# Kernel tuning notes

Measured on AMD Instinct MI355X. Metric: run time of the kernel, lower is better.

The kernel has to match this reference:

```python
import jax, jax.numpy as jnp
import numpy as np

EPS = 1e-09
TOP_K = 2
TEMPERATURE = 1.0


def setup_inputs() -> dict:
    key = jax.random.key(0)
    k1, k2, k3, k4 = jax.random.split(key, 4)
    B, T, H, C, E = 16, 8192, 256, 256, 16
    D = H + C          # router input dim = 512
    F = 2 * D          # hidden dim of router MLP = 1024
    inputs = jax.random.normal(k1, (B, T, H), dtype=jnp.float32)
    cond = jax.random.normal(k2, (B, T, C), dtype=jnp.float32)
    # router params (torch init: normal(0, 0.02) weights, zero bias)
    W1 = 0.02 * jax.random.normal(k3, (D, F), dtype=jnp.float32)
    b1 = jnp.zeros((F,), dtype=jnp.float32)
    W2 = 0.02 * jax.random.normal(k4, (F, E), dtype=jnp.float32)
    b2 = jnp.zeros((E,), dtype=jnp.float32)
    return {"inputs": inputs, "cond": cond, "W1": W1, "b1": b1, "W2": W2, "b2": b2}


def reference(inputs, cond, W1, b1, W2, b2):
    B, T, H = inputs.shape
    E = W2.shape[-1]
    # --- logits: concat(inputs, cond) -> Linear -> GELU(exact) -> Linear ---
    x = jnp.concatenate([inputs, cond], axis=-1).reshape(-1, H + cond.shape[-1])  # [N, D]
    h = jax.nn.gelu(x @ W1 + b1, approximate=False)                               # [N, F]
    logits = h @ W2 + b2                                                          # [N, E]
    # --- probabilities: max-subtract / temperature, softmax, clamp ---
    logits = (logits - jnp.max(logits, axis=-1, keepdims=True)) / TEMPERATURE
    probs = jax.nn.softmax(logits, axis=-1)
    probs = jnp.clip(probs, EPS, 1.0 - EPS)                                       # [N, E]
    # --- deterministic top-k selection (use_argmax / eval mode) ---
    top_vals, top_idx = jax.lax.top_k(probs, TOP_K)                               # [N, K]
    onehot = jax.nn.one_hot(top_idx, E, dtype=probs.dtype)                        # [N, K, E]
    router_mask = jnp.sum(onehot, axis=1)                                         # [N, E] 0/1
    router_probs = jnp.einsum('nke,nk->ne', onehot, top_vals)                     # scatter top-k probs
    # --- normalize selected probs ---
    router_probs = router_probs / jnp.sum(router_probs, axis=-1, keepdims=True)
    router_mask = router_mask.reshape(B, T, E)
    top_idx = top_idx.reshape(B, T, TOP_K)
    router_probs = router_probs.reshape(B, T, E)
    probs_full = probs.reshape(B, T, E)
    return (router_mask, top_idx, router_probs, probs_full)
```

## Files before the change

### kernel.cpp

```cpp
#include <hip/hip_runtime.h>
#include <math.h>

#define NTOK 131072
#define HDIM 256
#define DDIM 512
#define FDIM 1024
#define EDIM 16
#define TBLK 128
#define FCH  128
#define KST  32
#define HSS  68

#define WS_XL   134217728ULL
#define WS_W1H  268435456ULL
#define WS_W1L  269484032ULL
#define WS_NEED 270532608ULL

typedef __attribute__((ext_vector_type(8))) _Float16 v8h;
typedef __attribute__((ext_vector_type(4))) _Float16 v4h;
typedef __attribute__((ext_vector_type(4))) float v4f;

__device__ __forceinline__ void f2h2(float v, _Float16& h, _Float16& l) {
    h = (_Float16)v;
    l = (_Float16)(v - (float)h);
}

__device__ __forceinline__ void pack8(const float* u, v8h& hh, v8h& hl) {
    _Float16 h0,l0,h1,l1,h2,l2,h3,l3,h4,l4,h5,l5,h6,l6,h7,l7;
    f2h2(u[0],h0,l0); f2h2(u[1],h1,l1); f2h2(u[2],h2,l2); f2h2(u[3],h3,l3);
    f2h2(u[4],h4,l4); f2h2(u[5],h5,l5); f2h2(u[6],h6,l6); f2h2(u[7],h7,l7);
    hh[0]=h0; hh[1]=h1; hh[2]=h2; hh[3]=h3; hh[4]=h4; hh[5]=h5; hh[6]=h6; hh[7]=h7;
    hl[0]=l0; hl[1]=l1; hl[2]=l2; hl[3]=l3; hl[4]=l4; hl[5]=l5; hl[6]=l6; hl[7]=l7;
}

__device__ __forceinline__ void gl16(const void* g, void* l) {
    __builtin_amdgcn_global_load_lds(
        (const __attribute__((address_space(1))) void*)g,
        (__attribute__((address_space(3))) void*)l, 16, 0, 0);
}

__global__ __launch_bounds__(256, 4)
void prep_x(const float* __restrict__ inp, const float* __restrict__ cnd,
            _Float16* __restrict__ xh, _Float16* __restrict__ xl)
{
    const size_t g = (size_t)blockIdx.x * 256 + threadIdx.x;
    const int lane = (int)(g & 63);
    const int fg   = (int)((g >> 6) & 7);
    const int T    = (int)(g >> 9);
    const int tb = T >> 4, st = T & 15;
    const int tok = tb * TBLK + fg * 16 + (lane & 15);
    const int k   = st * KST + (lane >> 4) * 8;
    const float* src = (k < HDIM) ? (inp + (size_t)tok * HDIM + k)
                                  : (cnd + (size_t)tok * HDIM + (k - HDIM));
    float u[8];
    *(float4*)&u[0] = *(const float4*)(src);
    *(float4*)&u[4] = *(const float4*)(src + 4);
    v8h hh, hl;
    pack8(u, hh, hl);
    *(v8h*)(xh + g * 8) = hh;
    *(v8h*)(xl + g * 8) = hl;
}

__global__ __launch_bounds__(256, 4)
void prep_w1(const float* __restrict__ W1,
             _Float16* __restrict__ wh, _Float16* __restrict__ wl)
{
    const int g = blockIdx.x * 256 + threadIdx.x;
    const int lane = g & 63;
    const int K = (g >> 6) & 15;
    const int F = g >> 10;
    const int f  = F * 16 + (lane & 15);
    const int kb = K * KST + (lane >> 4) * 8;
    float u[8];
#pragma unroll
    for (int e = 0; e < 8; ++e)
        u[e] = W1[(size_t)(kb + e) * FDIM + f];
    v8h hh, hl;
    pack8(u, hh, hl);
    *(v8h*)(wh + (size_t)g * 8) = hh;
    *(v8h*)(wl + (size_t)g * 8) = hl;
}

__global__ __launch_bounds__(256, 2)
void router_mfma12(const _Float16* __restrict__ xh, const _Float16* __restrict__ xl,
                   const _Float16* __restrict__ w1h, const _Float16* __restrict__ w1l,
                   const float* __restrict__ b1,
                   const float* __restrict__ W2,
                   const float* __restrict__ b2,
                   float* __restrict__ out)
{
    __shared__ __align__(16) char smem[34816];
    _Float16* xs_h = (_Float16*)(smem);
    _Float16* xs_l = (_Float16*)(smem + 8192);
    _Float16* ws_h = (_Float16*)(smem + 16384);
    _Float16* ws_l = (_Float16*)(smem + 24576);
    _Float16* hs_h = (_Float16*)(smem);
    _Float16* hs_l = (_Float16*)(smem + 17408);

    const int tid  = threadIdx.x;
    const int lane = tid & 63;
    const int w    = tid >> 6;
    const int wr   = w >> 1;
    const int wf   = w & 1;
    const int l15  = lane & 15;
    const int l4   = lane >> 4;
    const int t0   = blockIdx.x * TBLK;

    const float b2v = b2[l15];
    v4f accL[2] = {{0.f,0.f,0.f,0.f},{0.f,0.f,0.f,0.f}};

    for (int fc = 0; fc < FDIM; fc += FCH) {
        v4f acc[4][4];
#pragma unroll
        for (int mf = 0; mf < 4; ++mf)
#pragma unroll
            for (int nf = 0; nf < 4; ++nf)
                acc[mf][nf] = (v4f){0.f,0.f,0.f,0.f};

        for (int st = 0; st < 16; ++st) {
            __syncthreads();
            {
                const char* sh = (const char*)(xh + ((size_t)blockIdx.x * 16 + st) * 4096);
                const char* sl = (const char*)(xl + ((size_t)blockIdx.x * 16 + st) * 4096);
                gl16(sh + tid * 16,        smem + tid * 16);
                gl16(sh + tid * 16 + 4096, smem + tid * 16 + 4096);
                gl16(sl + tid * 16,        smem + 8192 + tid * 16);
                gl16(sl + tid * 16 + 4096, smem + 8192 + tid * 16 + 4096);
                const size_t wb0 = (((size_t)((fc >> 4) + (tid >> 6)) * 16 + st) * 64
                                    + (tid & 63)) * 16;
                const size_t wb1 = (((size_t)((fc >> 4) + 4 + (tid >> 6)) * 16 + st) * 64
                                    + (tid & 63)) * 16;
                gl16((const char*)w1h + wb0, smem + 16384 + tid * 16);
                gl16((const char*)w1h + wb1, smem + 16384 + tid * 16 + 4096);
                gl16((const char*)w1l + wb0, smem + 24576 + tid * 16);
                gl16((const char*)w1l + wb1, smem + 24576 + tid * 16 + 4096);
            }
            __syncthreads();
            {
                v8h ah[4], al[4];
#pragma unroll
                for (int mf = 0; mf < 4; ++mf) {
                    const int aoff = ((4 * wr + mf) * 64 + lane) * 8;
                    ah[mf] = *(const v8h*)(xs_h + aoff);
                    al[mf] = *(const v8h*)(xs_l + aoff);
                }
#pragma unroll
                for (int nf = 0; nf < 4; ++nf) {
                    const int boff = ((4 * wf + nf) * 64 + lane) * 8;
                    const v8h bh = *(const v8h*)(ws_h + boff);
                    const v8h bl = *(const v8h*)(ws_l + boff);
#pragma unroll
                    for (int mf = 0; mf < 4; ++mf) {
                        acc[mf][nf] = __builtin_amdgcn_mfma_f32_16x16x32_f16(ah[mf], bh, acc[mf][nf], 0, 0, 0);
                        acc[mf][nf] = __builtin_amdgcn_mfma_f32_16x16x32_f16(al[mf], bh, acc[mf][nf], 0, 0, 0);
                        acc[mf][nf] = __builtin_amdgcn_mfma_f32_16x16x32_f16(ah[mf], bl, acc[mf][nf], 0, 0, 0);
                    }
                }
            }
        }
        __syncthreads();

        float b1v[4];
#pragma unroll
        for (int nf = 0; nf < 4; ++nf)
            b1v[nf] = b1[fc + 64 * wf + 16 * nf + l15];

#pragma unroll
        for (int h = 0; h < 2; ++h) {
            if (wf == h) {
#pragma unroll
                for (int mf = 0; mf < 4; ++mf)
#pragma unroll
                    for (int nf = 0; nf < 4; ++nf)
#pragma unroll
                        for (int r = 0; r < 4; ++r) {
                            const float v = acc[mf][nf][r] + b1v[nf];
                            const float gl = 0.5f * v * (1.0f + erff(v * 0.70710678118654752f));
                            _Float16 hh, hl;
                            f2h2(gl, hh, hl);
                            const int tok  = 64 * wr + 16 * mf + 4 * l4 + r;
                            const int fcol = 16 * nf + l15;
                            hs_h[tok * HSS + fcol] = hh;
                            hs_l[tok * HSS + fcol] = hl;
                        }
            }
            __syncthreads();
#pragma unroll
            for (int ks = 0; ks < 2; ++ks) {
                v8h vbh, vbl;
#pragma unroll
                for (int j = 0; j < 8; ++j) {
                    const float u = W2[(size_t)(fc + 64 * h + 32 * ks + 8 * l4 + j) * EDIM + l15];
                    _Float16 hh, hl;
                    f2h2(u, hh, hl);
                    vbh[j] = hh; vbl[j] = hl;
                }
#pragma unroll
                for (int mf2 = 0; mf2 < 2; ++mf2) {
                    const int aoff = (32 * w + 16 * mf2 + l15) * HSS + 32 * ks + 8 * l4;
                    const v8h vah = *(const v8h*)(hs_h + aoff);
                    const v8h val = *(const v8h*)(hs_l + aoff);
                    accL[mf2] = __builtin_amdgcn_mfma_f32_16x16x32_f16(vah, vbh, accL[mf2], 0, 0, 0);
                    accL[mf2] = __builtin_amdgcn_mfma_f32_16x16x32_f16(val, vbh, accL[mf2], 0, 0, 0);
                    accL[mf2] = __builtin_amdgcn_mfma_f32_16x16x32_f16(vah, vbl, accL[mf2], 0, 0, 0);
                }
            }
            if (h == 0) __syncthreads();
        }
    }

    float lg[8];
#pragma unroll
    for (int mf2 = 0; mf2 < 2; ++mf2)
#pragma unroll
        for (int r = 0; r < 4; ++r)
            lg[mf2 * 4 + r] = accL[mf2][r] + b2v;

    const int tx = l15;
#pragma unroll
    for (int i = 0; i < 8; ++i) {
        const int t = t0 + 32 * w + 16 * (i >> 2) + 4 * l4 + (i & 3);
        float mx = lg[i];
#pragma unroll
        for (int m = 1; m < 16; m <<= 1) mx = fmaxf(mx, __shfl_xor(mx, m, 64));
        float p = expf(lg[i] - mx);
        float s = p;
#pragma unroll
        for (int m = 1; m < 16; m <<= 1) s += __shfl_xor(s, m, 64);
        float pr = p / s;
        pr = fminf(fmaxf(pr, 1e-9f), 1.0f - 1e-9f);

        float v1 = pr; int i1 = tx;
#pragma unroll
        for (int m = 1; m < 16; m <<= 1) {
            const float vo = __shfl_xor(v1, m, 64);
            const int   io = __shfl_xor(i1, m, 64);
            if (vo > v1 || (vo == v1 && io < i1)) { v1 = vo; i1 = io; }
        }
        float v2 = (tx == i1) ? -1.0f : pr; int i2 = tx;
#pragma unroll
        for (int m = 1; m < 16; m <<= 1) {
            const float vo = __shfl_xor(v2, m, 64);
            const int   io = __shfl_xor(i2, m, 64);
            if (vo > v2 || (vo == v2 && io < i2)) { v2 = vo; i2 = io; }
        }
        const float rs = 1.0f / (v1 + v2);

        float* om  = out + (size_t)t * EDIM;
        float* orp = out + (size_t)NTOK * 18 + (size_t)t * EDIM;
        float* opf = out + (size_t)NTOK * 34 + (size_t)t * EDIM;
        om[tx]  = (tx == i1 || tx == i2) ? 1.0f : 0.0f;
        orp[tx] = (tx == i1) ? v1 * rs : ((tx == i2) ? v2 * rs : 0.0f);
        opf[tx] = pr;
        if (tx == 0) {
            float2* oi = (float2*)(out + (size_t)NTOK * 16 + (size_t)t * 2);
            *oi = make_float2((float)i1, (float)i2);
        }
    }
}

#define XST  40
#define HST  68
#define FCHB 64
__global__ __launch_bounds__(256, 2)
void router_mfma7(const float* __restrict__ inp,
                  const float* __restrict__ cnd,
                  const float* __restrict__ W1,
                  const float* __restrict__ b1,
                  const float* __restrict__ W2,
                  const float* __restrict__ b2,
                  float* __restrict__ out)
{
    __shared__ __align__(16) char smem[34816];
    _Float16* xs_h = (_Float16*)(smem);
    _Float16* xs_l = (_Float16*)(smem + 10240);
    _Float16* ws_h = (_Float16*)(smem + 20480);
    _Float16* ws_l = (_Float16*)(smem + 25600);
    float*    hs   = (float*)(smem);

    const int tid  = threadIdx.x;
    const int lane = tid & 63;
    const int w    = tid >> 6;
    const int wr   = w >> 1;
    const int wc   = w & 1;
    const int l15  = lane & 15;
    const int l4   = lane >> 4;
    const int t0   = blockIdx.x * TBLK;
    const int ty   = tid >> 4;
    const int tx   = tid & 15;
    const int kq   = tid & 7;
    const int xr   = tid >> 3;
    const int fcl  = tid & 63;
    const int kg   = tid >> 6;

    float lg[8];
    { const float bb = b2[tx];
#pragma unroll
      for (int i = 0; i < 8; ++i) lg[i] = bb; }

    for (int fc = 0; fc < FDIM; fc += FCHB) {
        v4f acc[4][2];
#pragma unroll
        for (int mf = 0; mf < 4; ++mf)
#pragma unroll
            for (int nf = 0; nf < 2; ++nf) acc[mf][nf] = (v4f){0.f,0.f,0.f,0.f};

        for (int st = 0; st < 16; ++st) {
            const int kc = st * KST;
            __syncthreads();
            {
                const float* src = (kc < HDIM) ? (inp + (size_t)t0 * HDIM + kc)
                                               : (cnd + (size_t)t0 * HDIM + (kc - HDIM));
#pragma unroll
                for (int p = 0; p < 4; ++p) {
                    const int row = xr + 32 * p;
                    const float4 v = *(const float4*)(src + (size_t)row * HDIM + kq * 4);
                    _Float16 h0,l0,h1,l1,h2,l2,h3,l3;
                    f2h2(v.x,h0,l0); f2h2(v.y,h1,l1); f2h2(v.z,h2,l2); f2h2(v.w,h3,l3);
                    v4h hh, hl;
                    hh[0]=h0; hh[1]=h1; hh[2]=h2; hh[3]=h3;
                    hl[0]=l0; hl[1]=l1; hl[2]=l2; hl[3]=l3;
                    *(v4h*)(xs_h + row * XST + kq * 4) = hh;
                    *(v4h*)(xs_l + row * XST + kq * 4) = hl;
                }
            }
#pragma unroll
            for (int s = 0; s < 2; ++s) {
                const int kb = 4 * kg + 16 * s;
                const float u0 = W1[(size_t)(kc + kb + 0) * FDIM + fc + fcl];
                const float u1 = W1[(size_t)(kc + kb + 1) * FDIM + fc + fcl];
                const float u2 = W1[(size_t)(kc + kb + 2) * FDIM + fc + fcl];
                const float u3 = W1[(size_t)(kc + kb + 3) * FDIM + fc + fcl];
                _Float16 h0,l0,h1,l1,h2,l2,h3,l3;
                f2h2(u0,h0,l0); f2h2(u1,h1,l1); f2h2(u2,h2,l2); f2h2(u3,h3,l3);
                v4h hh, hl;
                hh[0]=h0; hh[1]=h1; hh[2]=h2; hh[3]=h3;
                hl[0]=l0; hl[1]=l1; hl[2]=l2; hl[3]=l3;
                *(v4h*)(ws_h + fcl * XST + kb) = hh;
                *(v4h*)(ws_l + fcl * XST + kb) = hl;
            }
            __syncthreads();
            {
                v8h bh[2], bl[2];
#pragma unroll
                for (int nf = 0; nf < 2; ++nf) {
                    const int off = (32 * wc + 16 * nf + l15) * XST + 8 * l4;
                    bh[nf] = *(const v8h*)(ws_h + off);
                    bl[nf] = *(const v8h*)(ws_l + off);
                }
#pragma unroll
                for (int mf = 0; mf < 4; ++mf) {
                    const int off = (64 * wr + 16 * mf + l15) * XST + 8 * l4;
                    const v8h ah = *(const v8h*)(xs_h + off);
                    const v8h al = *(const v8h*)(xs_l + off);
#pragma unroll
                    for (int nf = 0; nf < 2; ++nf) {
                        acc[mf][nf] = __builtin_amdgcn_mfma_f32_16x16x32_f16(ah, bh[nf], acc[mf][nf], 0, 0, 0);
                        acc[mf][nf] = __builtin_amdgcn_mfma_f32_16x16x32_f16(al, bh[nf], acc[mf][nf], 0, 0, 0);
                        acc[mf][nf] = __builtin_amdgcn_mfma_f32_16x16x32_f16(ah, bl[nf], acc[mf][nf], 0, 0, 0);
                    }
                }
            }
        }
        __syncthreads();
        {
            float b1v[2];
#pragma unroll
            for (int nf = 0; nf < 2; ++nf) b1v[nf] = b1[fc + 32 * wc + 16 * nf + l15];
#pragma unroll
            for (int mf = 0; mf < 4; ++mf)
#pragma unroll
                for (int nf = 0; nf < 2; ++nf)
#pragma unroll
                    for (int r = 0; r < 4; ++r) {
                        const float v = acc[mf][nf][r] + b1v[nf];
                        const int tok  = 64 * wr + 16 * mf + 4 * l4 + r;
                        const int fcol = 32 * wc + 16 * nf + l15;
                        hs[tok * HST + fcol] = 0.5f * v * (1.0f + erff(v * 0.70710678118654752f));
                    }
        }
        __syncthreads();
#pragma unroll
        for (int jb = 0; jb < 16; ++jb) {
            const int jbs = (jb + 4 * l4) & 15;
            float w2v[4];
#pragma unroll
            for (int j = 0; j < 4; ++j)
                w2v[j] = W2[(size_t)(fc + jbs * 4 + j) * EDIM + tx];
#pragma unroll
            for (int i = 0; i < 8; ++i) {
                const float4 hv = *(const float4*)(hs + (ty * 8 + i) * HST + jbs * 4);
                lg[i] = fmaf(hv.x, w2v[0], lg[i]);
                lg[i] = fmaf(hv.y, w2v[1], lg[i]);
                lg[i] = fmaf(hv.z, w2v[2], lg[i]);
                lg[i] = fmaf(hv.w, w2v[3], lg[i]);
            }
        }
    }
#pragma unroll
    for (int i = 0; i < 8; ++i) {
        const int t = t0 + ty * 8 + i;
        float mx = lg[i];
#pragma unroll
        for (int m = 1; m < 16; m <<= 1) mx = fmaxf(mx, __shfl_xor(mx, m, 64));
        float p = expf(lg[i] - mx);
        float s = p;
#pragma unroll
        for (int m = 1; m < 16; m <<= 1) s += __shfl_xor(s, m, 64);
        float pr = p / s;
        pr = fminf(fmaxf(pr, 1e-9f), 1.0f - 1e-9f);
        float v1 = pr; int i1 = tx;
#pragma unroll
        for (int m = 1; m < 16; m <<= 1) {
            const float vo = __shfl_xor(v1, m, 64);
            const int   io = __shfl_xor(i1, m, 64);
            if (vo > v1 || (vo == v1 && io < i1)) { v1 = vo; i1 = io; }
        }
        float v2 = (tx == i1) ? -1.0f : pr; int i2 = tx;
#pragma unroll
        for (int m = 1; m < 16; m <<= 1) {
            const float vo = __shfl_xor(v2, m, 64);
            const int   io = __shfl_xor(i2, m, 64);
            if (vo > v2 || (vo == v2 && io < i2)) { v2 = vo; i2 = io; }
        }
        const float rs = 1.0f / (v1 + v2);
        float* om  = out + (size_t)t * EDIM;
        float* orp = out + (size_t)NTOK * 18 + (size_t)t * EDIM;
        float* opf = out + (size_t)NTOK * 34 + (size_t)t * EDIM;
        om[tx]  = (tx == i1 || tx == i2) ? 1.0f : 0.0f;
        orp[tx] = (tx == i1) ? v1 * rs : ((tx == i2) ? v2 * rs : 0.0f);
        opf[tx] = pr;
        if (tx == 0) {
            float2* oi = (float2*)(out + (size_t)NTOK * 16 + (size_t)t * 2);
            *oi = make_float2((float)i1, (float)i2);
        }
    }
}

extern "C" void kernel_launch(void* const* d_in, const int* in_sizes, int n_in,
                              void* d_out, int out_size, void* d_ws, size_t ws_size,
                              hipStream_t stream)
{
    const float* inp = (const float*)d_in[0];
    const float* cnd = (const float*)d_in[1];
    const float* W1  = (const float*)d_in[2];
    const float* b1  = (const float*)d_in[3];
    const float* W2  = (const float*)d_in[4];
    const float* b2  = (const float*)d_in[5];
    float* out = (float*)d_out;

    if (ws_size >= WS_NEED) {
        char* wsb = (char*)d_ws;
        _Float16* xh  = (_Float16*)(wsb);
        _Float16* xl  = (_Float16*)(wsb + WS_XL);
        _Float16* w1h = (_Float16*)(wsb + WS_W1H);
        _Float16* w1l = (_Float16*)(wsb + WS_W1L);
        hipLaunchKernelGGL(prep_x, dim3(32768), dim3(256), 0, stream, inp, cnd, xh, xl);
        hipLaunchKernelGGL(prep_w1, dim3(256), dim3(256), 0, stream, W1, w1h, w1l);
        hipLaunchKernelGGL(router_mfma12, dim3(NTOK / TBLK), dim3(256), 0, stream,
                           xh, xl, w1h, w1l, b1, W2, b2, out);
    } else {
        hipLaunchKernelGGL(router_mfma7, dim3(NTOK / TBLK), dim3(256), 0, stream,
                           inp, cnd, W1, b1, W2, b2, out);
    }
}
```

Measured before the change: 652.8 us.

## Double-buffer LDS tiles to overlap global loads with MFMA compute

Shared memory grows to two 32KB buffers, and the next K-step's x and W1 tiles are staged into the alternate buffer while MFMAs run on the current one. This replaces two barriers per step with one and is meant to hide global-to-LDS load latency behind compute. The cost is 64KB of LDS per block, which may cut occupancy relative to launch_bounds(256,2), and the hs epilogue still aliases buffer 0.

```diff
diff --git a/kernel.cpp b/kernel.cpp
--- a/kernel.cpp
+++ b/kernel.cpp
@@ -81,19 +81,37 @@
     *(v8h*)(wl + (size_t)g * 8) = hl;
 }
 
+__device__ __forceinline__ void stage_tiles(char* smem, int b, int tid,
+        const _Float16* xh, const _Float16* xl,
+        const _Float16* w1h, const _Float16* w1l,
+        int blk, int fc, int st)
+{
+    char* base = smem + b * 32768;
+    const char* sh = (const char*)(xh + ((size_t)blk * 16 + st) * 4096);
+    const char* sl = (const char*)(xl + ((size_t)blk * 16 + st) * 4096);
+    gl16(sh + tid * 16,        base + tid * 16);
+    gl16(sh + tid * 16 + 4096, base + tid * 16 + 4096);
+    gl16(sl + tid * 16,        base + 8192 + tid * 16);
+    gl16(sl + tid * 16 + 4096, base + 8192 + tid * 16 + 4096);
+    const size_t wb0 = (((size_t)((fc >> 4) + (tid >> 6)) * 16 + st) * 64
+                        + (tid & 63)) * 16;
+    const size_t wb1 = (((size_t)((fc >> 4) + 4 + (tid >> 6)) * 16 + st) * 64
+                        + (tid & 63)) * 16;
+    gl16((const char*)w1h + wb0, base + 16384 + tid * 16);
+    gl16((const char*)w1h + wb1, base + 16384 + tid * 16 + 4096);
+    gl16((const char*)w1l + wb0, base + 24576 + tid * 16);
+    gl16((const char*)w1l + wb1, base + 24576 + tid * 16 + 4096);
+}
+
 __global__ __launch_bounds__(256, 2)
-void router_mfma12(const _Float16* __restrict__ xh, const _Float16* __restrict__ xl,
+void router_mfma13(const _Float16* __restrict__ xh, const _Float16* __restrict__ xl,
                    const _Float16* __restrict__ w1h, const _Float16* __restrict__ w1l,
                    const float* __restrict__ b1,
                    const float* __restrict__ W2,
                    const float* __restrict__ b2,
                    float* __restrict__ out)
 {
-    __shared__ __align__(16) char smem[34816];
-    _Float16* xs_h = (_Float16*)(smem);
-    _Float16* xs_l = (_Float16*)(smem + 8192);
-    _Float16* ws_h = (_Float16*)(smem + 16384);
-    _Float16* ws_l = (_Float16*)(smem + 24576);
+    __shared__ __align__(16) char smem[65536];
     _Float16* hs_h = (_Float16*)(smem);
     _Float16* hs_l = (_Float16*)(smem + 17408);
 
@@ -109,6 +127,7 @@
     const float b2v = b2[l15];
     v4f accL[2] = {{0.f,0.f,0.f,0.f},{0.f,0.f,0.f,0.f}};
 
+    int cur = 0;
     for (int fc = 0; fc < FDIM; fc += FCH) {
         v4f acc[4][4];
 #pragma unroll
@@ -117,26 +136,19 @@
             for (int nf = 0; nf < 4; ++nf)
                 acc[mf][nf] = (v4f){0.f,0.f,0.f,0.f};
 
+        __syncthreads();
+        stage_tiles(smem, cur, tid, xh, xl, w1h, w1l, blockIdx.x, fc, 0);
+        __syncthreads();
+
         for (int st = 0; st < 16; ++st) {
-            __syncthreads();
+            if (st < 15)
+                stage_tiles(smem, cur ^ 1, tid, xh, xl, w1h, w1l,
+                            blockIdx.x, fc, st + 1);
             {
-                const char* sh = (const char*)(xh + ((size_t)blockIdx.x * 16 + st) * 4096);
-                const char* sl = (const char*)(xl + ((size_t)blockIdx.x * 16 + st) * 4096);
-                gl16(sh + tid * 16,        smem + tid * 16);
-                gl16(sh + tid * 16 + 4096, smem + tid * 16 + 4096);
-                gl16(sl + tid * 16,        smem + 8192 + tid * 16);
-                gl16(sl + tid * 16 + 4096, smem + 8192 + tid * 16 + 4096);
-                const size_t wb0 = (((size_t)((fc >> 4) + (tid >> 6)) * 16 + st) * 64
-                                    + (tid & 63)) * 16;
-                const size_t wb1 = (((size_t)((fc >> 4) + 4 + (tid >> 6)) * 16 + st) * 64
-                                    + (tid & 63)) * 16;
-                gl16((const char*)w1h + wb0, smem + 16384 + tid * 16);
-                gl16((const char*)w1h + wb1, smem + 16384 + tid * 16 + 4096);
-                gl16((const char*)w1l + wb0, smem + 24576 + tid * 16);
-                gl16((const char*)w1l + wb1, smem + 24576 + tid * 16 + 4096);
-            }
-            __syncthreads();
-            {
+                const _Float16* xs_h = (const _Float16*)(smem + cur * 32768);
+                const _Float16* xs_l = (const _Float16*)(smem + cur * 32768 + 8192);
+                const _Float16* ws_h = (const _Float16*)(smem + cur * 32768 + 16384);
+                const _Float16* ws_l = (const _Float16*)(smem + cur * 32768 + 24576);
                 v8h ah[4], al[4];
 #pragma unroll
                 for (int mf = 0; mf < 4; ++mf) {
@@ -157,8 +169,9 @@
                     }
                 }
             }
-        }
-        __syncthreads();
+            __syncthreads();
+            cur ^= 1;
+        }
 
         float b1v[4];
 #pragma unroll
@@ -457,7 +470,7 @@
         _Float16* w1l = (_Float16*)(wsb + WS_W1L);
         hipLaunchKernelGGL(prep_x, dim3(32768), dim3(256), 0, stream, inp, cnd, xh, xl);
         hipLaunchKernelGGL(prep_w1, dim3(256), dim3(256), 0, stream, W1, w1h, w1l);
-        hipLaunchKernelGGL(router_mfma12, dim3(NTOK / TBLK), dim3(256), 0, stream,
+        hipLaunchKernelGGL(router_mfma13, dim3(NTOK / TBLK), dim3(256), 0, stream,
                            xh, xl, w1h, w1l, b1, W2, b2, out);
     } else {
         hipLaunchKernelGGL(router_mfma7, dim3(NTOK / TBLK), dim3(256), 0, stream,
```

New measurement: 632.7 us. -3.1%, faster.
